# Kernel tuning notes

Hardware: AMD Instinct MI355X
Metric: run time of the kernel (lower is better)

Reference implementation:

```python
import jax, jax.numpy as jnp
import numpy as np

V, E, F, H, L = 512, 32768, 8, 128, 3


def setup_inputs() -> dict:
    key = jax.random.key(0)
    ks = jax.random.split(key, 10)
    adj_matrix = jax.random.normal(ks[0], (V, V, F), dtype=jnp.float32)
    edges = jax.random.randint(ks[1], (E, 2), 0, V, dtype=jnp.int64)
    emb_w = jax.random.normal(ks[2], (H, F), dtype=jnp.float32) / np.sqrt(F)
    msg_w1 = jax.random.normal(ks[3], (L, H, H), dtype=jnp.float32) / np.sqrt(H)
    msg_w2 = jax.random.normal(ks[4], (L, H, H), dtype=jnp.float32) / np.sqrt(H)
    msg_w3 = jax.random.normal(ks[5], (L, H, H), dtype=jnp.float32) / np.sqrt(H)
    gru_w_ih = jax.random.normal(ks[6], (3 * H, 2 * H), dtype=jnp.float32) / np.sqrt(2 * H)
    gru_w_hh = jax.random.normal(ks[7], (3 * H, H), dtype=jnp.float32) / np.sqrt(H)
    gru_b_ih = jax.random.normal(ks[8], (3 * H,), dtype=jnp.float32) * 0.01
    gru_b_hh = jax.random.normal(ks[9], (3 * H,), dtype=jnp.float32) * 0.01
    return {"adj_matrix": adj_matrix, "edges": edges, "emb_w": emb_w,
            "msg_w1": msg_w1, "msg_w2": msg_w2, "msg_w3": msg_w3,
            "gru_w_ih": gru_w_ih, "gru_w_hh": gru_w_hh,
            "gru_b_ih": gru_b_ih, "gru_b_hh": gru_b_hh}


def _message_passing(x, u, v, w1, w2, w3):
    # x: (V,V,h). For edge (u,v): e_in = masked mean of column u (row v zeroed),
    # e_out = masked mean of column v (row u zeroed); N = count_nonzero/h (if 0 -> 1).
    h_dim = x.shape[-1]
    col_sum = jnp.sum(x, axis=0)                 # (V,h): sum over rows of each column
    nnz_col = jnp.sum(x != 0, axis=(0, 2))       # (V,): nonzero elems per column
    x_uv = x[u, v]                               # (E,h)
    x_vu = x[v, u]                               # (E,h)
    # incoming: column u with row v zeroed
    n_in = (nnz_col[u] - jnp.sum(x_vu != 0, axis=-1)).astype(x.dtype) / h_dim
    n_in = jnp.where(n_in == 0, jnp.ones_like(n_in), n_in)
    e_in = (col_sum[u] - x_vu) / n_in[:, None]
    # outgoing: column v with row u zeroed
    n_out = (nnz_col[v] - jnp.sum(x_uv != 0, axis=-1)).astype(x.dtype) / h_dim
    n_out = jnp.where(n_out == 0, jnp.ones_like(n_out), n_out)
    e_out = (col_sum[v] - x_uv) / n_out[:, None]
    msg = jax.nn.relu(x_uv @ w1.T + e_in @ w2.T + e_out @ w3.T)  # (E,h)
    return x.at[u, v].set(msg)


def _gru(x_seq, w_ih, w_hh, b_ih, b_hh):
    # x_seq: (B,T,2h), batch_first GRU, h0 = 0. PyTorch gate order: r,z,n.
    B = x_seq.shape[0]
    h_dim = w_hh.shape[1]
    xi = jnp.einsum('bti,gi->btg', x_seq, w_ih) + b_ih  # (B,T,3h), precompute input proj

    def step(h_prev, xt):
        gh = h_prev @ w_hh.T + b_hh
        xr, xz, xn = jnp.split(xt, 3, axis=-1)
        hr, hz, hn = jnp.split(gh, 3, axis=-1)
        r = jax.nn.sigmoid(xr + hr)
        z = jax.nn.sigmoid(xz + hz)
        n = jnp.tanh(xn + r * hn)
        h_new = (1 - z) * n + z * h_prev
        return h_new, h_new

    h0 = jnp.zeros((B, h_dim), dtype=x_seq.dtype)
    _, ys = jax.lax.scan(step, h0, jnp.swapaxes(xi, 0, 1))  # (T,B,h)
    return jnp.swapaxes(ys, 0, 1)


def reference(adj_matrix, edges, emb_w, msg_w1, msg_w2, msg_w3,
              gru_w_ih, gru_w_hh, gru_b_ih, gru_b_hh):
    u, v = edges[:, 0], edges[:, 1]
    x = jnp.einsum('abf,hf->abh', adj_matrix, emb_w)  # (V,V,h)
    for layer in range(msg_w1.shape[0]):
        m = _message_passing(x, u, v, msg_w1[layer], msg_w2[layer], msg_w3[layer])
        x = _gru(jnp.concatenate([m, x], axis=-1), gru_w_ih, gru_w_hh, gru_b_ih, gru_b_hh)
    return x
```

## Files before the change

### kernel.cpp

```cpp
#include <hip/hip_runtime.h>

#define VN 512
#define EN 32768
#define FN 8
#define HN 128
#define G3 384
#define LN 3
#define TP 16
#define NROWS (VN*VN)
#define XIPAD 388

typedef _Float16 f16x8 __attribute__((ext_vector_type(8)));
typedef float f32x4  __attribute__((ext_vector_type(4)));

__device__ __forceinline__ unsigned short f2h(float f) {
    _Float16 h = (_Float16)f;
    return __builtin_bit_cast(unsigned short, h);
}
__device__ __forceinline__ float h2f(unsigned short u) {
    return (float)__builtin_bit_cast(_Float16, u);
}
__device__ __forceinline__ float fexp2(float x) {
    float r; asm("v_exp_f32 %0, %1" : "=v"(r) : "v"(x)); return r;
}
__device__ __forceinline__ float frcp(float x) {
    float r; asm("v_rcp_f32 %0, %1" : "=v"(r) : "v"(x)); return r;
}
__device__ __forceinline__ float fsigmoid(float x) {
    return frcp(1.f + fexp2(x * -1.44269504089f));
}
__device__ __forceinline__ float ftanh(float x) {
    return 1.f - 2.f * frcp(1.f + fexp2(x * 2.88539008178f));
}

__global__ void k_fill(int* __restrict__ p, int val, int n) {
    int i = blockIdx.x * 256 + threadIdx.x;
    if (i < n) p[i] = val;
}

__global__ void k_edges(const void* __restrict__ raw, int* __restrict__ uo, int* __restrict__ vo) {
    const int* r32 = (const int*)raw;
    const long long* r64 = (const long long*)raw;
    int acc = 0;
    #pragma unroll
    for (int i = 1; i < 128; i += 2) acc |= r32[i];
    bool is64 = (acc == 0);
    int e = blockIdx.x * 256 + threadIdx.x;
    if (e < EN) {
        int u, v;
        if (is64) { u = (int)r64[2*e]; v = (int)r64[2*e+1]; }
        else      { u = r32[2*e];      v = r32[2*e+1]; }
        uo[e] = u; vo[e] = v;
    }
}

__global__ void k_pack(const float* __restrict__ w1, const float* __restrict__ w2,
                       const float* __restrict__ w3, const float* __restrict__ wih,
                       const float* __restrict__ whh,
                       unsigned short* __restrict__ wsF, unsigned short* __restrict__ whF,
                       unsigned short* __restrict__ wlF, unsigned short* __restrict__ wcF) {
    int t = blockIdx.x * 256 + threadIdx.x;
    if (t < 3*8*12*64*8) {
        int e = t & 7, lane = (t >> 3) & 63;
        int frag = t >> 9;
        int kt = frag % 12;
        int rem = frag / 12;
        int nt = rem & 7;
        int l  = rem >> 3;
        int k  = kt*32 + (lane >> 4)*8 + e;
        int gc = nt*16 + (lane & 15);
        const float* w = (k < 128) ? w1 : (k < 256 ? w2 : w3);
        wcF[t] = f2h(w[((long)l*128 + gc)*128 + (k & 127)]);
    }
    if (t < 24*4*64*8) {
        int e = t & 7, lane = (t >> 3) & 63, kt = (t >> 9) & 3, nt = t >> 11;
        int k  = kt*32 + (lane >> 4)*8 + e;
        int gc = nt*16 + (lane & 15);
        wsF[t] = f2h(wih[gc*256 + k] + wih[gc*256 + 128 + k]);
        whF[t] = f2h(whh[gc*HN + k]);
        wlF[t] = f2h(wih[gc*256 + k]);
    }
}

__global__ void k_map(const int* __restrict__ uA, const int* __restrict__ vA, int* __restrict__ map) {
    int e = blockIdx.x * 256 + threadIdx.x;
    if (e < EN) atomicMax(&map[uA[e]*VN + vA[e]], e);
}

__global__ __launch_bounds__(256) void k_embed(const float* __restrict__ adj,
                                               const float* __restrict__ emb,
                                               float* __restrict__ x) {
    __shared__ float semb[HN][FN];
    __shared__ float sadj[2][FN];
    int tid = threadIdx.x;
    for (int i = tid; i < HN*FN; i += 256) semb[i/FN][i%FN] = emb[i];
    if (tid < 16) sadj[tid>>3][tid&7] = adj[(long)blockIdx.x*16 + tid];
    __syncthreads();
    int p = tid >> 7;
    int h = tid & 127;
    float acc = 0.f;
    #pragma unroll
    for (int f = 0; f < FN; f++) acc += sadj[p][f]*semb[h][f];
    long row = (long)blockIdx.x*2 + p;
    x[row*HN + h] = acc;
}

__global__ __launch_bounds__(512) void k_colsum(const float* __restrict__ x,
                                                float* __restrict__ colsum, int* __restrict__ nnz) {
    int b = blockIdx.x;
    int tid = threadIdx.x;
    int h = tid & 127, q = tid >> 7;
    float s = 0.f; int c = 0;
    for (int a = q*128; a < q*128 + 128; a++) {
        float v = x[((long)a*VN + b)*HN + h];
        s += v; c += (v != 0.f) ? 1 : 0;
    }
    __shared__ float ss[4][128];
    __shared__ int sc[8];
    ss[q][h] = s;
    #pragma unroll
    for (int off = 32; off; off >>= 1) c += __shfl_down(c, off);
    if ((tid & 63) == 0) sc[tid>>6] = c;
    __syncthreads();
    if (tid < 128) colsum[b*HN + tid] = ss[0][tid]+ss[1][tid]+ss[2][tid]+ss[3][tid];
    if (tid == 0) { int t = 0; for (int i = 0; i < 8; i++) t += sc[i]; nnz[b] = t; }
}

__global__ __launch_bounds__(256) void k_edgein(const float* __restrict__ x,
    const int* __restrict__ uA, const int* __restrict__ vA,
    const float* __restrict__ colsum, const int* __restrict__ nnz, float* __restrict__ in3) {
    int w = threadIdx.x >> 6;
    int lane = threadIdx.x & 63;
    int e = blockIdx.x*4 + w;
    int u = uA[e], v = vA[e];
    const float* xuv = x + ((long)u*VN + v)*HN;
    const float* xvu = x + ((long)v*VN + u)*HN;
    float xu0 = xuv[lane], xu1 = xuv[lane+64];
    float xv0 = xvu[lane], xv1 = xvu[lane+64];
    int cnt_vu = __popcll(__ballot(xv0 != 0.f)) + __popcll(__ballot(xv1 != 0.f));
    int cnt_uv = __popcll(__ballot(xu0 != 0.f)) + __popcll(__ballot(xu1 != 0.f));
    float nin  = (float)(nnz[u] - cnt_vu) * (1.f/128.f); if (nin  == 0.f) nin  = 1.f;
    float nout = (float)(nnz[v] - cnt_uv) * (1.f/128.f); if (nout == 0.f) nout = 1.f;
    float* o = in3 + (long)e*G3;
    o[lane]        = xu0;  o[lane+64]      = xu1;
    o[128+lane]    = (colsum[u*HN+lane]    - xv0)/nin;
    o[128+lane+64] = (colsum[u*HN+lane+64] - xv1)/nin;
    o[256+lane]    = (colsum[v*HN+lane]    - xu0)/nout;
    o[256+lane+64] = (colsum[v*HN+lane+64] - xu1)/nout;
}

#define MF16(A,B,C) __builtin_amdgcn_mfma_f32_16x16x32_f16((A),(B),(C),0,0,0)
#define Z4 ((f32x4){0.f,0.f,0.f,0.f})

__global__ __launch_bounds__(512) void k_msgcorr(
    const float* __restrict__ in3,
    const unsigned short* __restrict__ wcF, const unsigned short* __restrict__ wlF,
    float* __restrict__ corr) {
    const int g = threadIdx.x;
    const int wv = g >> 6;
    const int lane = g & 63;
    const int r16 = lane & 15;
    const int kgrp = lane >> 4;
    const long m0 = (long)blockIdx.x * 16;

    __shared__ unsigned short Dh[16][136];
    __shared__ unsigned short Dl[16][136];

    f32x4 pacc[2];
    pacc[0] = Z4; pacc[1] = Z4;
    #pragma unroll
    for (int kt = 0; kt < 12; kt++) {
        const float* xs = &in3[(m0 + r16)*G3 + kt*32 + kgrp*8];
        float4 v0 = *(const float4*)xs;
        float4 v1 = *(const float4*)(xs + 4);
        float vv[8] = {v0.x,v0.y,v0.z,v0.w,v1.x,v1.y,v1.z,v1.w};
        f16x8 H, L;
        #pragma unroll
        for (int j = 0; j < 8; j++) {
            _Float16 h = (_Float16)vv[j];
            H[j] = h;
            L[j] = (_Float16)(vv[j] - (float)h);
        }
        f16x8 bF = *(const f16x8*)&wcF[(((long)wv*12 + kt)*64 + lane)*8];
        const int p = kt & 1;
        pacc[p] = MF16(H, bF, pacc[p]);
        pacc[p] = MF16(L, bF, pacc[p]);
    }
    const int c = wv*16 + r16;
    #pragma unroll
    for (int r = 0; r < 4; r++) {
        int m = kgrp*4 + r;
        float mv = fmaxf(pacc[0][r] + pacc[1][r], 0.f) - in3[(m0 + m)*G3 + c];
        unsigned short hi = f2h(mv);
        Dh[m][c] = hi;
        Dl[m][c] = f2h(mv - h2f(hi));
    }
    __syncthreads();

    f32x4 cacc[3];
    cacc[0] = cacc[1] = cacc[2] = Z4;
    #pragma unroll
    for (int kt = 0; kt < 4; kt++) {
        f16x8 ah = *(const f16x8*)&Dh[r16][kt*32 + kgrp*8];
        f16x8 al = *(const f16x8*)&Dl[r16][kt*32 + kgrp*8];
        #pragma unroll
        for (int j = 0; j < 3; j++) {
            f16x8 bF = *(const f16x8*)&wlF[(((long)(wv*3 + j)*4 + kt)*64 + lane)*8];
            cacc[j] = MF16(ah, bF, cacc[j]);
            cacc[j] = MF16(al, bF, cacc[j]);
        }
    }
    #pragma unroll
    for (int j = 0; j < 3; j++) {
        int n = (wv*3 + j)*16 + r16;
        #pragma unroll
        for (int r = 0; r < 4; r++)
            corr[(m0 + kgrp*4 + r)*G3 + n] = cacc[j][r];
    }
}


#define STAGE(ROWBASE) do { \
    int rs_ = g >> 8, row_ = (g >> 4) & 15, cg_ = g & 15; \
    const float* xs_ = &x[((long)(a0 + rs_*256)*VN + (ROWBASE) + row_)*HN + cg_*8]; \
    float4 v0_ = *(const float4*)xs_; \
    float4 v1_ = *(const float4*)(xs_ + 4); \
    f16x8 H_; \
    H_[0] = (_Float16)v0_.x; H_[1] = (_Float16)v0_.y; \
    H_[2] = (_Float16)v0_.z; H_[3] = (_Float16)v0_.w; \
    H_[4] = (_Float16)v1_.x; H_[5] = (_Float16)v1_.y; \
    H_[6] = (_Float16)v1_.z; H_[7] = (_Float16)v1_.w; \
    int slot_ = cg_ ^ row_; \
    *(f16x8*)&xSh[rs_][row_][slot_*8] = H_; \
} while(0)

#define XI_PAIR(GI, KT) do { \
    f16x8 bF_ = *(const f16x8*)&wsF[(((long)((GI)*8 + wv)*4 + (KT))*64 + lane)*8]; \
    int slot_ = ((KT)*4 + kgrp) ^ r16; \
    f16x8 A0_ = *(const f16x8*)&xSh[0][r16][slot_*8]; \
    f16x8 A1_ = *(const f16x8*)&xSh[1][r16][slot_*8]; \
    xacc0##GI = MF16(A0_, bF_, xacc0##GI); \
    xacc1##GI = MF16(A1_, bF_, xacc1##GI); \
} while(0)

#define XI_STORE() do { \
    _Pragma("unroll") \
    for (int r_ = 0; r_ < 4; ++r_) { \
        xiP[0][kgrp*4 + r_][c]        = xacc00[r_] + biR; \
        xiP[0][kgrp*4 + r_][HN + c]   = xacc01[r_] + biZ; \
        xiP[0][kgrp*4 + r_][2*HN + c] = xacc02[r_] + biN; \
        xiP[1][kgrp*4 + r_][c]        = xacc10[r_] + biR; \
        xiP[1][kgrp*4 + r_][HN + c]   = xacc11[r_] + biZ; \
        xiP[1][kgrp*4 + r_][2*HN + c] = xacc12[r_] + biN; \
    } \
} while(0)

#define CORR_ADD() do { if (g < G3) { \
    for (int rs_ = 0; rs_ < 2; ++rs_) \
        for (int t_ = 0; t_ < TP; ++t_) { \
            int e_ = eS[rs_][t_]; \
            if (e_ >= 0) xiP[rs_][t_][g] += corr[(long)e_*G3 + g]; \
        } } } while(0)

#define STEP(T) do { \
    const int arow_ = r16 & 1; \
    f16x8 hA0_ = *(const f16x8*)&hSh[cur][arow_][0*32 + kgrp*8]; \
    f16x8 hA1_ = *(const f16x8*)&hSh[cur][arow_][1*32 + kgrp*8]; \
    f16x8 hA2_ = *(const f16x8*)&hSh[cur][arow_][2*32 + kgrp*8]; \
    f16x8 hA3_ = *(const f16x8*)&hSh[cur][arow_][3*32 + kgrp*8]; \
    f32x4 gr0_ = Z4, gr1_ = Z4, gz0_ = Z4, gz1_ = Z4, gn0_ = Z4, gn1_ = Z4; \
    __builtin_amdgcn_s_setprio(1); \
    gr0_ = MF16(hA0_, wH[0], gr0_); \
    gr1_ = MF16(hA1_, wH[1], gr1_); \
    gr0_ = MF16(hA2_, wH[2], gr0_); \
    gr1_ = MF16(hA3_, wH[3], gr1_); \
    gz0_ = MF16(hA0_, wH[4], gz0_); \
    gz1_ = MF16(hA1_, wH[5], gz1_); \
    gz0_ = MF16(hA2_, wH[6], gz0_); \
    gz1_ = MF16(hA3_, wH[7], gz1_); \
    gn0_ = MF16(hA0_, wH[8], gn0_); \
    gn1_ = MF16(hA1_, wH[9], gn1_); \
    gn0_ = MF16(hA2_, wH[10], gn0_); \
    gn1_ = MF16(hA3_, wH[11], gn1_); \
    __builtin_amdgcn_s_setprio(0); \
    float sR_ = gr0_[0] + gr1_[0], tR_ = gr0_[1] + gr1_[1]; \
    float sZ_ = gz0_[0] + gz1_[0], tZ_ = gz0_[1] + gz1_[1]; \
    float sN_ = gn0_[0] + gn1_[0], tN_ = gn0_[1] + gn1_[1]; \
    float mR_ = __int_as_float(__builtin_amdgcn_ds_swizzle(__float_as_int(tR_), 0x401F)); \
    float mZ_ = __int_as_float(__builtin_amdgcn_ds_swizzle(__float_as_int(tZ_), 0x401F)); \
    float mN_ = __int_as_float(__builtin_amdgcn_ds_swizzle(__float_as_int(tN_), 0x401F)); \
    float vR_ = (lane < 16) ? sR_ : mR_; \
    float vZ_ = (lane < 16) ? sZ_ : mZ_; \
    float vN_ = (lane < 16) ? sN_ : mN_; \
    if (lane < 32) { \
        int rs_ = lane >> 4; \
        float xr_ = xiP[rs_][T][c]; \
        float xz_ = xiP[rs_][T][HN + c]; \
        float xn_ = xiP[rs_][T][2*HN + c]; \
        float r_ = fsigmoid(xr_ + vR_ + br); \
        float z_ = fsigmoid(xz_ + vZ_ + bz); \
        float n_ = ftanh(xn_ + r_*(vN_ + bn)); \
        float h_ = (1.f - z_)*n_ + z_*hprev; \
        hprev = h_; \
        hOut[rs_][T][c] = h_; \
        hSh[cur ^ 1][rs_][c] = f2h(h_); \
    } \
    cur ^= 1; \
    __syncthreads(); \
} while(0)

__global__ __launch_bounds__(512) void k_scanf(
    float* __restrict__ x,
    const unsigned short* __restrict__ wsF, const unsigned short* __restrict__ whF,
    const float* __restrict__ bih, const float* __restrict__ bhh,
    const float* __restrict__ corr, const int* __restrict__ map) {
    const int g = threadIdx.x;
    const int a0 = blockIdx.x;
    const int wv = g >> 6;
    const int lane = g & 63;
    const int r16 = lane & 15;
    const int kgrp = lane >> 4;

    __shared__ float xiP[2][TP][XIPAD];
    __shared__ unsigned short xSh[2][TP][HN];
    __shared__ unsigned short hSh[2][2][HN];
    __shared__ float hOut[2][TP][HN];
    __shared__ int eS[2][TP];

    f16x8 wH[12];
    #pragma unroll
    for (int gi = 0; gi < 3; gi++)
        #pragma unroll
        for (int kt = 0; kt < 4; kt++) {
            long bidx = (((long)(gi*8 + wv)*4 + kt)*64 + lane)*8;
            wH[gi*4+kt] = *(const f16x8*)&whF[bidx];
        }

    const int c = wv*16 + r16;
    const float br = bhh[c],  bz = bhh[HN + c],  bn = bhh[2*HN + c];
    const float biR = bih[c], biZ = bih[HN + c], biN = bih[2*HN + c];
    float hprev = 0.f;

    if (g < 2*HN) ((unsigned short*)hSh)[g] = 0;
    int cur = 0;

    STAGE(0);
    __syncthreads();

    for (int p0 = 0; p0 < VN; p0 += TP) {
        const bool hasnext = (p0 + TP) < VN;

        if (p0 > 0) {
            int pp = p0 - TP;
            for (int idx = g; idx < 2*TP*32; idx += 512) {
                int rs = idx >> 9, j = idx & 511, t = j >> 5, c4 = j & 31;
                *(float4*)&x[((long)(a0 + rs*256)*VN + pp + t)*HN + c4*4] =
                    *(const float4*)&hOut[rs][t][c4*4];
            }
        }
        if (g < 32) eS[g >> 4][g & 15] = map[(long)(a0 + (g >> 4)*256)*VN + p0 + (g & 15)];
        {
            f32x4 xacc00 = Z4, xacc01 = Z4, xacc02 = Z4;
            f32x4 xacc10 = Z4, xacc11 = Z4, xacc12 = Z4;
            XI_PAIR(0,0); XI_PAIR(0,1); XI_PAIR(0,2); XI_PAIR(0,3);
            XI_PAIR(1,0); XI_PAIR(1,1); XI_PAIR(1,2); XI_PAIR(1,3);
            XI_PAIR(2,0); XI_PAIR(2,1); XI_PAIR(2,2); XI_PAIR(2,3);
            XI_STORE();
        }
        __syncthreads();

        if (hasnext) STAGE(p0 + TP);
        CORR_ADD();
        __syncthreads();

        STEP(0);  STEP(1);  STEP(2);  STEP(3);
        STEP(4);  STEP(5);  STEP(6);  STEP(7);
        STEP(8);  STEP(9);  STEP(10); STEP(11);
        STEP(12); STEP(13); STEP(14); STEP(15);
    }
    {
        int pp = VN - TP;
        for (int idx = g; idx < 2*TP*32; idx += 512) {
            int rs = idx >> 9, j = idx & 511, t = j >> 5, c4 = j & 31;
            *(float4*)&x[((long)(a0 + rs*256)*VN + pp + t)*HN + c4*4] =
                *(const float4*)&hOut[rs][t][c4*4];
        }
    }
}

extern "C" void kernel_launch(void* const* d_in, const int* in_sizes, int n_in,
                              void* d_out, int out_size, void* d_ws, size_t ws_size,
                              hipStream_t stream) {
    const float* adj   = (const float*)d_in[0];
    const void*  edges = d_in[1];
    const float* emb   = (const float*)d_in[2];
    const float* w1    = (const float*)d_in[3];
    const float* w2    = (const float*)d_in[4];
    const float* w3    = (const float*)d_in[5];
    const float* wih   = (const float*)d_in[6];
    const float* whh   = (const float*)d_in[7];
    const float* bih   = (const float*)d_in[8];
    const float* bhh   = (const float*)d_in[9];

    float* x = (float*)d_out;

    char* p = (char*)d_ws;
    auto alloc = [&](size_t bytes) { char* r = p; p += (bytes + 255) & ~255UL; return r; };
    float* in3    = (float*)alloc((size_t)EN*G3*4);
    float* corr   = (float*)alloc((size_t)EN*G3*4);
    float* colsum = (float*)alloc((size_t)VN*HN*4);
    int*   nnz    = (int*)  alloc((size_t)VN*4);
    int*   map    = (int*)  alloc((size_t)NROWS*4);
    int*   uA     = (int*)  alloc((size_t)EN*4);
    int*   vA     = (int*)  alloc((size_t)EN*4);
    unsigned short* wsF = (unsigned short*)alloc((size_t)24*4*64*8*2);
    unsigned short* whF = (unsigned short*)alloc((size_t)24*4*64*8*2);
    unsigned short* wlF = (unsigned short*)alloc((size_t)24*4*64*8*2);
    unsigned short* wcF = (unsigned short*)alloc((size_t)3*8*12*64*8*2);

    k_edges<<<EN/256, 256, 0, stream>>>(edges, uA, vA);
    k_pack<<<(3*8*12*64*8 + 255)/256, 256, 0, stream>>>(w1, w2, w3, wih, whh,
        wsF, whF, wlF, wcF);
    k_fill<<<NROWS/256, 256, 0, stream>>>(map, -1, NROWS);
    k_map<<<EN/256, 256, 0, stream>>>(uA, vA, map);
    k_embed<<<NROWS/2, 256, 0, stream>>>(adj, emb, x);

    for (int l = 0; l < LN; l++) {
        k_colsum<<<VN, 512, 0, stream>>>(x, colsum, nnz);
        k_edgein<<<EN/4, 256, 0, stream>>>(x, uA, vA, colsum, nnz, in3);
        k_msgcorr<<<EN/16, 512, 0, stream>>>(in3, wcF + (long)l*8*12*64*8, wlF, corr);
        k_scanf<<<VN/2, 512, 0, stream>>>(x, wsF, whF, bih, bhh, corr, map);
    }
}
```

Baseline: 1.412 ms.

## Fuse edge-input gather into message MFMA kernel via swizzled shared memory

Merges the edge-input gather kernel into the message/correction MFMA kernel. Each block now builds its 16 edge rows of the input directly in shared memory as hi/lo fp16 pairs, using an XOR swizzle to avoid bank conflicts. This drops the 48 MB in3 global round trip and one launch per layer. In exchange it adds about 24 KB of LDS per block, which may lower occupancy. It also rebuilds x_uv from the fp16 hi+lo split instead of the exact fp32 value.

```diff
diff --git a/kernel.cpp b/kernel.cpp
--- a/kernel.cpp
+++ b/kernel.cpp
@@ -126,34 +126,13 @@
     if (tid == 0) { int t = 0; for (int i = 0; i < 8; i++) t += sc[i]; nnz[b] = t; }
 }
 
-__global__ __launch_bounds__(256) void k_edgein(const float* __restrict__ x,
-    const int* __restrict__ uA, const int* __restrict__ vA,
-    const float* __restrict__ colsum, const int* __restrict__ nnz, float* __restrict__ in3) {
-    int w = threadIdx.x >> 6;
-    int lane = threadIdx.x & 63;
-    int e = blockIdx.x*4 + w;
-    int u = uA[e], v = vA[e];
-    const float* xuv = x + ((long)u*VN + v)*HN;
-    const float* xvu = x + ((long)v*VN + u)*HN;
-    float xu0 = xuv[lane], xu1 = xuv[lane+64];
-    float xv0 = xvu[lane], xv1 = xvu[lane+64];
-    int cnt_vu = __popcll(__ballot(xv0 != 0.f)) + __popcll(__ballot(xv1 != 0.f));
-    int cnt_uv = __popcll(__ballot(xu0 != 0.f)) + __popcll(__ballot(xu1 != 0.f));
-    float nin  = (float)(nnz[u] - cnt_vu) * (1.f/128.f); if (nin  == 0.f) nin  = 1.f;
-    float nout = (float)(nnz[v] - cnt_uv) * (1.f/128.f); if (nout == 0.f) nout = 1.f;
-    float* o = in3 + (long)e*G3;
-    o[lane]        = xu0;  o[lane+64]      = xu1;
-    o[128+lane]    = (colsum[u*HN+lane]    - xv0)/nin;
-    o[128+lane+64] = (colsum[u*HN+lane+64] - xv1)/nin;
-    o[256+lane]    = (colsum[v*HN+lane]    - xu0)/nout;
-    o[256+lane+64] = (colsum[v*HN+lane+64] - xu1)/nout;
-}
-
 #define MF16(A,B,C) __builtin_amdgcn_mfma_f32_16x16x32_f16((A),(B),(C),0,0,0)
 #define Z4 ((f32x4){0.f,0.f,0.f,0.f})
 
-__global__ __launch_bounds__(512) void k_msgcorr(
-    const float* __restrict__ in3,
+__global__ __launch_bounds__(512) void k_fused(
+    const float* __restrict__ x,
+    const int* __restrict__ uA, const int* __restrict__ vA,
+    const float* __restrict__ colsum, const int* __restrict__ nnz,
     const unsigned short* __restrict__ wcF, const unsigned short* __restrict__ wlF,
     float* __restrict__ corr) {
     const int g = threadIdx.x;
@@ -163,37 +142,70 @@
     const int kgrp = lane >> 4;
     const long m0 = (long)blockIdx.x * 16;
 
+    __shared__ unsigned short i3h[16][G3];
+    __shared__ unsigned short i3l[16][G3];
     __shared__ unsigned short Dh[16][136];
     __shared__ unsigned short Dl[16][136];
 
+    #pragma unroll
+    for (int ei = 0; ei < 2; ei++) {
+        const int row = wv*2 + ei;
+        const int e = (int)m0 + row;
+        int u = uA[e], v = vA[e];
+        const float* xuv = x + ((long)u*VN + v)*HN;
+        const float* xvu = x + ((long)v*VN + u)*HN;
+        float xu0 = xuv[lane], xu1 = xuv[lane+64];
+        float xv0 = xvu[lane], xv1 = xvu[lane+64];
+        int cnt_vu = __popcll(__ballot(xv0 != 0.f)) + __popcll(__ballot(xv1 != 0.f));
+        int cnt_uv = __popcll(__ballot(xu0 != 0.f)) + __popcll(__ballot(xu1 != 0.f));
+        float nin  = (float)(nnz[u] - cnt_vu) * (1.f/128.f); if (nin  == 0.f) nin  = 1.f;
+        float nout = (float)(nnz[v] - cnt_uv) * (1.f/128.f); if (nout == 0.f) nout = 1.f;
+        float vals[6];
+        int   ks[6];
+        vals[0] = xu0;                                 ks[0] = lane;
+        vals[1] = xu1;                                 ks[1] = lane + 64;
+        vals[2] = (colsum[u*HN+lane]    - xv0)/nin;    ks[2] = 128 + lane;
+        vals[3] = (colsum[u*HN+lane+64] - xv1)/nin;    ks[3] = 128 + lane + 64;
+        vals[4] = (colsum[v*HN+lane]    - xu0)/nout;   ks[4] = 256 + lane;
+        vals[5] = (colsum[v*HN+lane+64] - xu1)/nout;   ks[5] = 256 + lane + 64;
+        #pragma unroll
+        for (int j = 0; j < 6; j++) {
+            int k = ks[j];
+            int g8 = k >> 3;
+            int addr = ((g8 & 48) | ((g8 & 15) ^ row))*8 + (k & 7);
+            unsigned short hi = f2h(vals[j]);
+            i3h[row][addr] = hi;
+            i3l[row][addr] = f2h(vals[j] - h2f(hi));
+        }
+    }
+    __syncthreads();
+
     f32x4 pacc[2];
     pacc[0] = Z4; pacc[1] = Z4;
     #pragma unroll
     for (int kt = 0; kt < 12; kt++) {
-        const float* xs = &in3[(m0 + r16)*G3 + kt*32 + kgrp*8];
-        float4 v0 = *(const float4*)xs;
-        float4 v1 = *(const float4*)(xs + 4);
-        float vv[8] = {v0.x,v0.y,v0.z,v0.w,v1.x,v1.y,v1.z,v1.w};
-        f16x8 H, L;
-        #pragma unroll
-        for (int j = 0; j < 8; j++) {
-            _Float16 h = (_Float16)vv[j];
-            H[j] = h;
-            L[j] = (_Float16)(vv[j] - (float)h);
-        }
+        int g8 = kt*4 + kgrp;
+        int addr = ((g8 & 48) | ((g8 & 15) ^ r16))*8;
+        f16x8 ah = *(const f16x8*)&i3h[r16][addr];
+        f16x8 al = *(const f16x8*)&i3l[r16][addr];
         f16x8 bF = *(const f16x8*)&wcF[(((long)wv*12 + kt)*64 + lane)*8];
         const int p = kt & 1;
-        pacc[p] = MF16(H, bF, pacc[p]);
-        pacc[p] = MF16(L, bF, pacc[p]);
+        pacc[p] = MF16(ah, bF, pacc[p]);
+        pacc[p] = MF16(al, bF, pacc[p]);
     }
     const int c = wv*16 + r16;
-    #pragma unroll
-    for (int r = 0; r < 4; r++) {
-        int m = kgrp*4 + r;
-        float mv = fmaxf(pacc[0][r] + pacc[1][r], 0.f) - in3[(m0 + m)*G3 + c];
-        unsigned short hi = f2h(mv);
-        Dh[m][c] = hi;
-        Dl[m][c] = f2h(mv - h2f(hi));
+    {
+        int g8c = c >> 3;
+        #pragma unroll
+        for (int r = 0; r < 4; r++) {
+            int m = kgrp*4 + r;
+            int addr = ((g8c ^ m) & 15)*8 + (c & 7);
+            float xuv_v = h2f(i3h[m][addr]) + h2f(i3l[m][addr]);
+            float mv = fmaxf(pacc[0][r] + pacc[1][r], 0.f) - xuv_v;
+            unsigned short hi = f2h(mv);
+            Dh[m][c] = hi;
+            Dl[m][c] = f2h(mv - h2f(hi));
+        }
     }
     __syncthreads();
 
@@ -406,7 +418,6 @@
 
     char* p = (char*)d_ws;
     auto alloc = [&](size_t bytes) { char* r = p; p += (bytes + 255) & ~255UL; return r; };
-    float* in3    = (float*)alloc((size_t)EN*G3*4);
     float* corr   = (float*)alloc((size_t)EN*G3*4);
     float* colsum = (float*)alloc((size_t)VN*HN*4);
     int*   nnz    = (int*)  alloc((size_t)VN*4);
@@ -427,8 +438,8 @@
 
     for (int l = 0; l < LN; l++) {
         k_colsum<<<VN, 512, 0, stream>>>(x, colsum, nnz);
-        k_edgein<<<EN/4, 256, 0, stream>>>(x, uA, vA, colsum, nnz, in3);
-        k_msgcorr<<<EN/16, 512, 0, stream>>>(in3, wcF + (long)l*8*12*64*8, wlF, corr);
+        k_fused<<<EN/16, 512, 0, stream>>>(x, uA, vA, colsum, nnz,
+                                           wcF + (long)l*8*12*64*8, wlF, corr);
         k_scanf<<<VN/2, 512, 0, stream>>>(x, wsF, whF, bih, bhh, corr, map);
     }
 }
```

Measured after the change: 1.296 ms. 8.2% less time.
